# Kernel tuning notes

Measured on AMD Instinct MI355X. Metric: run time of the kernel, lower is better.

Reference implementation:

```python
import jax, jax.numpy as jnp
import numpy as np

N_NODES = 100000
N_EDGES = 3200000
D_IN = 256
D_OUT = 256


def setup_inputs() -> dict:
    key = jax.random.key(0)
    k1, k2, k3, k4, k5 = jax.random.split(key, 5)
    x = jax.random.normal(k1, (N_NODES, D_IN), dtype=jnp.float32)
    weight = jax.random.normal(k2, (D_IN, D_OUT), dtype=jnp.float32)
    edge_rows = jax.random.randint(k3, (N_EDGES,), 0, N_NODES, dtype=jnp.int32)
    edge_cols = jax.random.randint(k4, (N_EDGES,), 0, N_NODES, dtype=jnp.int32)
    edge_vals = jax.random.uniform(k5, (N_EDGES,), dtype=jnp.float32)
    return {"x": x, "weight": weight, "edge_rows": edge_rows,
            "edge_cols": edge_cols, "edge_vals": edge_vals}


def reference(x, weight, edge_rows, edge_cols, edge_vals):
    # GraphConvolution forward (eval mode, dense features, no bias):
    #   xw  = x @ W                      [N, D_OUT]
    #   out = relu(A_sparse @ xw)        A given as COO edge list
    xw = x @ weight  # [N, D_OUT]
    msgs = edge_vals[:, None] * xw[edge_cols]  # gather source features, scale
    agg = jax.ops.segment_sum(msgs, edge_rows, num_segments=N_NODES)
    return jax.nn.relu(agg)
```

## Files before the change

### kernel.cpp

```cpp
#include <hip/hip_runtime.h>
#include <hip/hip_bf16.h>

#define N_NODES 100000
#define N_EDGES 3200000
#define D 256
#define RSH 7
#define RPB 128
#define NB ((N_NODES + RPB - 1) / RPB)
#define FILL_CH 8192
#define NBLK_E ((N_EDGES + FILL_CH - 1) / FILL_CH)

typedef __attribute__((ext_vector_type(8))) short short8;
typedef __attribute__((ext_vector_type(4))) float floatx4;

__device__ __forceinline__ unsigned short f32_to_bf16_rne(float f) {
    unsigned int u = __float_as_uint(f);
    u += 0x7FFFu + ((u >> 16) & 1u);
    return (unsigned short)(u >> 16);
}
__device__ __forceinline__ float bf16_bits_to_f32(unsigned short b) {
    return __uint_as_float(((unsigned int)b) << 16);
}
__device__ __forceinline__ float blo(unsigned int x) { return __uint_as_float(x << 16); }
__device__ __forceinline__ float bhi(unsigned int x) { return __uint_as_float(x & 0xFFFF0000u); }

__global__ __launch_bounds__(256) void convert_w_k(const float* __restrict__ w,
                                                   unsigned short* __restrict__ wsw) {
    int t = blockIdx.x * 256 + threadIdx.x;
    int j     = t & 7;
    int lane  = (t >> 3) & 63;
    int kstep = (t >> 9) & 7;
    int ntile = t >> 12;
    int k = kstep * 32 + (lane >> 4) * 8 + j;
    int n = ntile * 16 + (lane & 15);
    wsw[t] = f32_to_bf16_rne(w[k * D + n]);
}

__global__ __launch_bounds__(256) void gemm_xw_k(const float* __restrict__ x,
                                                 const unsigned short* __restrict__ wsw,
                                                 unsigned short* __restrict__ xwb) {
    __shared__ uint4 wlds[8192];
    const int tid = threadIdx.x;
#pragma unroll
    for (int i = 0; i < 32; ++i) {
        int idx = i * 256 + tid;
        wlds[idx] = ((const uint4*)wsw)[idx];
    }
    __syncthreads();

    const int lane = tid & 63;
    const int wave = tid >> 6;
    const int q    = lane >> 4;
    const int ml   = lane & 15;
    const long rowBase = (long)blockIdx.x * 64 + wave * 16;
    long arow = rowBase + ml;
    if (arow >= N_NODES) arow = 0;
    const float* xr = x + arow * (long)D;

    floatx4 acc[16];
#pragma unroll
    for (int i = 0; i < 16; ++i) acc[i] = (floatx4){0.f, 0.f, 0.f, 0.f};

    const short8* wfrag = (const short8*)wlds;

#pragma unroll
    for (int ks = 0; ks < 8; ++ks) {
        const float4 a0 = *(const float4*)(xr + ks * 32 + q * 8);
        const float4 a1 = *(const float4*)(xr + ks * 32 + q * 8 + 4);
        short8 af;
        af[0] = (short)f32_to_bf16_rne(a0.x);
        af[1] = (short)f32_to_bf16_rne(a0.y);
        af[2] = (short)f32_to_bf16_rne(a0.z);
        af[3] = (short)f32_to_bf16_rne(a0.w);
        af[4] = (short)f32_to_bf16_rne(a1.x);
        af[5] = (short)f32_to_bf16_rne(a1.y);
        af[6] = (short)f32_to_bf16_rne(a1.z);
        af[7] = (short)f32_to_bf16_rne(a1.w);
#pragma unroll
        for (int nt = 0; nt < 16; ++nt) {
            acc[nt] = __builtin_amdgcn_mfma_f32_16x16x32_bf16(
                af, wfrag[(nt * 8 + ks) * 64 + lane], acc[nt], 0, 0, 0);
        }
    }

#pragma unroll
    for (int nt = 0; nt < 16; ++nt) {
#pragma unroll
        for (int r = 0; r < 4; ++r) {
            long orow = rowBase + q * 4 + r;
            if (orow < N_NODES)
                xwb[orow * (long)D + nt * 16 + ml] = f32_to_bf16_rne(acc[nt][r]);
        }
    }
}

__global__ __launch_bounds__(256) void zero_counts_k(int* __restrict__ counts) {
    int i = blockIdx.x * 256 + threadIdx.x;
    if (i < NB) counts[i] = 0;
}

__global__ __launch_bounds__(256) void bhist_k(const int* __restrict__ erow,
                                               int* __restrict__ counts) {
    __shared__ int h[NB];
    const int tid = threadIdx.x;
    for (int i = tid; i < NB; i += 256) h[i] = 0;
    __syncthreads();
    const int s = blockIdx.x * FILL_CH;
    const int e = min(s + FILL_CH, N_EDGES);
    for (int i = s + tid; i < e; i += 256) atomicAdd(&h[erow[i] >> RSH], 1);
    __syncthreads();
    for (int i = tid; i < NB; i += 256)
        if (h[i] > 0) atomicAdd(&counts[i], h[i]);
}

__global__ __launch_bounds__(1024) void bscan_k(const int* __restrict__ counts,
                                                int* __restrict__ bbase,
                                                int* __restrict__ bcursor) {
    __shared__ int sc[1024];
    const int t = threadIdx.x;
    int v = (t < NB) ? counts[t] : 0;
    sc[t] = v;
    __syncthreads();
    for (int o = 1; o < 1024; o <<= 1) {
        int add = (t >= o) ? sc[t - o] : 0;
        __syncthreads();
        sc[t] += add;
        __syncthreads();
    }
    int excl = sc[t] - v;
    if (t < NB) { bbase[t] = excl; bcursor[t] = excl; }
    if (t == NB - 1) bbase[NB] = sc[t];
}

__global__ __launch_bounds__(256) void binfill_k(const int* __restrict__ erow,
                                                 const int* __restrict__ ecol,
                                                 const float* __restrict__ eval,
                                                 int* __restrict__ bcursor,
                                                 unsigned long long* __restrict__ recs) {
    __shared__ int h[NB];
    __shared__ int lcur[NB];
    const int tid = threadIdx.x;
    for (int i = tid; i < NB; i += 256) h[i] = 0;
    __syncthreads();
    const int s = blockIdx.x * FILL_CH;
    const int e = min(s + FILL_CH, N_EDGES);
    for (int i = s + tid; i < e; i += 256) atomicAdd(&h[erow[i] >> RSH], 1);
    __syncthreads();
    for (int i = tid; i < NB; i += 256) {
        int cnt = h[i];
        lcur[i] = (cnt > 0) ? atomicAdd(&bcursor[i], cnt) : 0;
    }
    __syncthreads();
    for (int i = s + tid; i < e; i += 256) {
        int r = erow[i];
        int b = r >> RSH;
        int pos = atomicAdd(&lcur[b], 1);
        unsigned long long rec =
            ((unsigned long long)(r & (RPB - 1)) << 33) |
            ((unsigned long long)f32_to_bf16_rne(eval[i]) << 17) |
            (unsigned int)ecol[i];
        recs[pos] = rec;
    }
}

__global__ __launch_bounds__(256) void bsort_k(const int* __restrict__ bbase,
                                               const unsigned long long* __restrict__ recs,
                                               int* __restrict__ offsets,
                                               unsigned int* __restrict__ cs,
                                               unsigned short* __restrict__ vs) {
    __shared__ int hist[RPB];
    __shared__ int cur[RPB];
    __shared__ int sc[RPB];
    const int t = threadIdx.x;
    const int b = blockIdx.x;
    const int base = bbase[b];
    const int endp = bbase[b + 1];

    if (t < RPB) hist[t] = 0;
    __syncthreads();
    for (int i = base + t; i < endp; i += 256)
        atomicAdd(&hist[(int)(recs[i] >> 33)], 1);
    __syncthreads();

    if (t < RPB) sc[t] = hist[t];
    __syncthreads();
    for (int o = 1; o < RPB; o <<= 1) {
        int add = (t >= o && t < RPB) ? sc[t - o] : 0;
        __syncthreads();
        if (t < RPB) sc[t] += add;
        __syncthreads();
    }
    if (t < RPB) {
        int excl = sc[t] - hist[t];
        cur[t] = excl;
        int r = (b << RSH) + t;
        if (r <= N_NODES) offsets[r] = base + excl;
    }
    __syncthreads();

    for (int i = base + t; i < endp; i += 256) {
        unsigned long long rec = recs[i];
        int rl = (int)(rec >> 33);
        int pos = base + atomicAdd(&cur[rl], 1);
        cs[pos] = (unsigned int)(rec & 0x1FFFFu);
        vs[pos] = (unsigned short)((rec >> 17) & 0xFFFFu);
    }
}

__global__ __launch_bounds__(256) void aggregate_k(const unsigned short* __restrict__ xwb,
                                                   const int* __restrict__ offsets,
                                                   const unsigned int* __restrict__ cs,
                                                   const unsigned short* __restrict__ vs,
                                                   float* __restrict__ out) {
    const int wave = threadIdx.x >> 6;
    const int lane = threadIdx.x & 63;
    const int r = blockIdx.x * 4 + wave;
    if (r >= N_NODES) return;

    const int start = offsets[r];
    const int end   = offsets[r + 1];
    const int half  = lane >> 5;
    const int hl    = lane & 31;

    float acc[8];
#pragma unroll
    for (int k = 0; k < 8; ++k) acc[k] = 0.f;

    for (int jb = start; jb < end; jb += 64) {
        int j = jb + lane;
        unsigned int c = 0;
        float v = 0.f;
        if (j < end) {
            c = cs[j];
            v = bf16_bits_to_f32(vs[j]);
        }
        const int cnt = min(64, end - jb);
        const int pairs = (cnt + 1) >> 1;
        int t = 0;
        for (; t + 4 <= pairs; t += 4) {
            uint4 q0, q1, q2, q3;
            float b0, b1, b2, b3;
#define SLOT(s, qv, bv)                                                        \
            {                                                                  \
                int src = 2 * (t + (s)) + half;                                \
                int srcc = min(src, cnt - 1);                                  \
                unsigned int bc = (unsigned int)__shfl((int)c, srcc);          \
                float bb = __shfl(v, srcc);                                    \
                bv = (src < cnt) ? bb : 0.f;                                   \
                qv = ((const uint4*)(xwb + (size_t)bc * D))[hl];               \
            }
            SLOT(0, q0, b0)
            SLOT(1, q1, b1)
            SLOT(2, q2, b2)
            SLOT(3, q3, b3)
#undef SLOT
#define FMA8(qv, bv)                                                           \
            acc[0] += bv * blo(qv.x); acc[1] += bv * bhi(qv.x);                \
            acc[2] += bv * blo(qv.y); acc[3] += bv * bhi(qv.y);                \
            acc[4] += bv * blo(qv.z); acc[5] += bv * bhi(qv.z);                \
            acc[6] += bv * blo(qv.w); acc[7] += bv * bhi(qv.w);
            FMA8(q0, b0)
            FMA8(q1, b1)
            FMA8(q2, b2)
            FMA8(q3, b3)
#undef FMA8
        }
        for (; t < pairs; ++t) {
            int src = 2 * t + half;
            int srcc = min(src, cnt - 1);
            unsigned int bc = (unsigned int)__shfl((int)c, srcc);
            float bb = __shfl(v, srcc);
            float bv = (src < cnt) ? bb : 0.f;
            uint4 q = ((const uint4*)(xwb + (size_t)bc * D))[hl];
            acc[0] += bv * blo(q.x); acc[1] += bv * bhi(q.x);
            acc[2] += bv * blo(q.y); acc[3] += bv * bhi(q.y);
            acc[4] += bv * blo(q.z); acc[5] += bv * bhi(q.z);
            acc[6] += bv * blo(q.w); acc[7] += bv * bhi(q.w);
        }
    }

#pragma unroll
    for (int k = 0; k < 8; ++k) acc[k] += __shfl_xor(acc[k], 32);

    const int s = lane >> 1;
    const int par = lane & 1;
    float4 o;
    {
        float a0 = __shfl(acc[0], s), b0 = __shfl(acc[4], s);
        float a1 = __shfl(acc[1], s), b1 = __shfl(acc[5], s);
        float a2 = __shfl(acc[2], s), b2 = __shfl(acc[6], s);
        float a3 = __shfl(acc[3], s), b3 = __shfl(acc[7], s);
        o.x = par ? b0 : a0;
        o.y = par ? b1 : a1;
        o.z = par ? b2 : a2;
        o.w = par ? b3 : a3;
    }
    o.x = fmaxf(o.x, 0.f);
    o.y = fmaxf(o.y, 0.f);
    o.z = fmaxf(o.z, 0.f);
    o.w = fmaxf(o.w, 0.f);
    ((float4*)(out + (size_t)r * D))[lane] = o;
}

extern "C" void kernel_launch(void* const* d_in, const int* in_sizes, int n_in,
                              void* d_out, int out_size, void* d_ws, size_t ws_size,
                              hipStream_t stream) {
    const float* x    = (const float*)d_in[0];
    const float* w    = (const float*)d_in[1];
    const int*   erow = (const int*)d_in[2];
    const int*   ecol = (const int*)d_in[3];
    const float* eval = (const float*)d_in[4];
    float* out = (float*)d_out;

    char* p = (char*)d_ws;
    auto align = [](size_t v) { return (v + 255) & ~(size_t)255; };

    unsigned short* xwb = (unsigned short*)p;
    p += align((size_t)N_NODES * D * sizeof(unsigned short));
    unsigned short* wsw = (unsigned short*)p;
    p += align((size_t)D * D * sizeof(unsigned short));
    int* bcounts = (int*)p;  p += align((size_t)NB * sizeof(int));
    int* bbase   = (int*)p;  p += align((size_t)(NB + 1) * sizeof(int));
    int* bcursor = (int*)p;  p += align((size_t)NB * sizeof(int));
    unsigned long long* recs = (unsigned long long*)p;
    p += align((size_t)N_EDGES * sizeof(unsigned long long));
    unsigned int*   cs = (unsigned int*)p;    p += align((size_t)N_EDGES * 4);
    unsigned short* vs = (unsigned short*)p;  p += align((size_t)N_EDGES * 2);
    int* offsets = (int*)p;  p += align((size_t)(N_NODES + 1) * sizeof(int));

    convert_w_k<<<(D * D) / 256, 256, 0, stream>>>(w, wsw);
    gemm_xw_k<<<(N_NODES + 63) / 64, 256, 0, stream>>>(x, wsw, xwb);
    zero_counts_k<<<(NB + 255) / 256, 256, 0, stream>>>(bcounts);
    bhist_k<<<NBLK_E, 256, 0, stream>>>(erow, bcounts);
    bscan_k<<<1, 1024, 0, stream>>>(bcounts, bbase, bcursor);
    binfill_k<<<NBLK_E, 256, 0, stream>>>(erow, ecol, eval, bcursor, recs);
    bsort_k<<<NB, 256, 0, stream>>>(bbase, recs, offsets, cs, vs);
    aggregate_k<<<(N_NODES + 3) / 4, 256, 0, stream>>>(xwb, offsets, cs, vs, out);
}
```

Baseline: 609.7 us.

## Enlarge GEMM blocks, deepen aggregate gather unroll, replace zero kernel with memset

The GEMM kernel now runs 512-thread blocks covering 128 rows, so the 128 KB bf16 weight tile loaded into LDS is reused by twice as many waves. The aggregation inner loop now issues eight unmasked row gathers per iteration over full pairs, with a 4-wide step and a masked scalar tail, and the outer and inner loops are kept rolled. This aims for more loads in flight and less per-slot clamping and masking. The bucket-count zeroing kernel is replaced by hipMemsetAsync. The costs are higher register pressure in the aggregate loop and fewer GEMM blocks resident per CU because of the large LDS footprint.

```diff
diff --git a/kernel.cpp b/kernel.cpp
--- a/kernel.cpp
+++ b/kernel.cpp
@@ -36,14 +36,14 @@
     wsw[t] = f32_to_bf16_rne(w[k * D + n]);
 }
 
-__global__ __launch_bounds__(256) void gemm_xw_k(const float* __restrict__ x,
+__global__ __launch_bounds__(512) void gemm_xw_k(const float* __restrict__ x,
                                                  const unsigned short* __restrict__ wsw,
                                                  unsigned short* __restrict__ xwb) {
     __shared__ uint4 wlds[8192];
     const int tid = threadIdx.x;
 #pragma unroll
-    for (int i = 0; i < 32; ++i) {
-        int idx = i * 256 + tid;
+    for (int i = 0; i < 16; ++i) {
+        int idx = i * 512 + tid;
         wlds[idx] = ((const uint4*)wsw)[idx];
     }
     __syncthreads();
@@ -52,7 +52,7 @@
     const int wave = tid >> 6;
     const int q    = lane >> 4;
     const int ml   = lane & 15;
-    const long rowBase = (long)blockIdx.x * 64 + wave * 16;
+    const long rowBase = (long)blockIdx.x * 128 + wave * 16;
     long arow = rowBase + ml;
     if (arow >= N_NODES) arow = 0;
     const float* xr = x + arow * (long)D;
@@ -94,11 +94,6 @@
     }
 }
 
-__global__ __launch_bounds__(256) void zero_counts_k(int* __restrict__ counts) {
-    int i = blockIdx.x * 256 + threadIdx.x;
-    if (i < NB) counts[i] = 0;
-}
-
 __global__ __launch_bounds__(256) void bhist_k(const int* __restrict__ erow,
                                                int* __restrict__ counts) {
     __shared__ int h[NB];
@@ -226,6 +221,7 @@
 #pragma unroll
     for (int k = 0; k < 8; ++k) acc[k] = 0.f;
 
+#pragma unroll 1
     for (int jb = start; jb < end; jb += 64) {
         int j = jb + lane;
         unsigned int c = 0;
@@ -236,35 +232,41 @@
         }
         const int cnt = min(64, end - jb);
         const int pairs = (cnt + 1) >> 1;
+        const int hp = cnt >> 1;
         int t = 0;
-        for (; t + 4 <= pairs; t += 4) {
+
+#define FMA8(qv, bv)                                                           \
+        acc[0] += bv * blo(qv.x); acc[1] += bv * bhi(qv.x);                    \
+        acc[2] += bv * blo(qv.y); acc[3] += bv * bhi(qv.y);                    \
+        acc[4] += bv * blo(qv.z); acc[5] += bv * bhi(qv.z);                    \
+        acc[6] += bv * blo(qv.w); acc[7] += bv * bhi(qv.w);
+#define SLOTF(s, qv, bv)                                                       \
+        {                                                                      \
+            int src = 2 * (t + (s)) + half;                                    \
+            unsigned int bc = (unsigned int)__shfl((int)c, src);               \
+            bv = __shfl(v, src);                                               \
+            qv = ((const uint4*)(xwb + (size_t)bc * D))[hl];                   \
+        }
+
+#pragma unroll 1
+        for (; t + 8 <= hp; t += 8) {
+            uint4 q0, q1, q2, q3, q4, q5, q6, q7;
+            float b0, b1, b2, b3, b4, b5, b6, b7;
+            SLOTF(0, q0, b0) SLOTF(1, q1, b1) SLOTF(2, q2, b2) SLOTF(3, q3, b3)
+            SLOTF(4, q4, b4) SLOTF(5, q5, b5) SLOTF(6, q6, b6) SLOTF(7, q7, b7)
+            FMA8(q0, b0) FMA8(q1, b1) FMA8(q2, b2) FMA8(q3, b3)
+            FMA8(q4, b4) FMA8(q5, b5) FMA8(q6, b6) FMA8(q7, b7)
+        }
+        if (t + 4 <= hp) {
             uint4 q0, q1, q2, q3;
             float b0, b1, b2, b3;
-#define SLOT(s, qv, bv)                                                        \
-            {                                                                  \
-                int src = 2 * (t + (s)) + half;                                \
-                int srcc = min(src, cnt - 1);                                  \
-                unsigned int bc = (unsigned int)__shfl((int)c, srcc);          \
-                float bb = __shfl(v, srcc);                                    \
-                bv = (src < cnt) ? bb : 0.f;                                   \
-                qv = ((const uint4*)(xwb + (size_t)bc * D))[hl];               \
-            }
-            SLOT(0, q0, b0)
-            SLOT(1, q1, b1)
-            SLOT(2, q2, b2)
-            SLOT(3, q3, b3)
-#undef SLOT
-#define FMA8(qv, bv)                                                           \
-            acc[0] += bv * blo(qv.x); acc[1] += bv * bhi(qv.x);                \
-            acc[2] += bv * blo(qv.y); acc[3] += bv * bhi(qv.y);                \
-            acc[4] += bv * blo(qv.z); acc[5] += bv * bhi(qv.z);                \
-            acc[6] += bv * blo(qv.w); acc[7] += bv * bhi(qv.w);
-            FMA8(q0, b0)
-            FMA8(q1, b1)
-            FMA8(q2, b2)
-            FMA8(q3, b3)
-#undef FMA8
-        }
+            SLOTF(0, q0, b0) SLOTF(1, q1, b1) SLOTF(2, q2, b2) SLOTF(3, q3, b3)
+            FMA8(q0, b0) FMA8(q1, b1) FMA8(q2, b2) FMA8(q3, b3)
+            t += 4;
+        }
+#undef SLOTF
+
+#pragma unroll 1
         for (; t < pairs; ++t) {
             int src = 2 * t + half;
             int srcc = min(src, cnt - 1);
@@ -272,11 +274,9 @@
             float bb = __shfl(v, srcc);
             float bv = (src < cnt) ? bb : 0.f;
             uint4 q = ((const uint4*)(xwb + (size_t)bc * D))[hl];
-            acc[0] += bv * blo(q.x); acc[1] += bv * bhi(q.x);
-            acc[2] += bv * blo(q.y); acc[3] += bv * bhi(q.y);
-            acc[4] += bv * blo(q.z); acc[5] += bv * bhi(q.z);
-            acc[6] += bv * blo(q.w); acc[7] += bv * bhi(q.w);
-        }
+            FMA8(q, bv)
+        }
+#undef FMA8
     }
 
 #pragma unroll
@@ -329,8 +329,8 @@
     int* offsets = (int*)p;  p += align((size_t)(N_NODES + 1) * sizeof(int));
 
     convert_w_k<<<(D * D) / 256, 256, 0, stream>>>(w, wsw);
-    gemm_xw_k<<<(N_NODES + 63) / 64, 256, 0, stream>>>(x, wsw, xwb);
-    zero_counts_k<<<(NB + 255) / 256, 256, 0, stream>>>(bcounts);
+    gemm_xw_k<<<(N_NODES + 127) / 128, 512, 0, stream>>>(x, wsw, xwb);
+    hipMemsetAsync(bcounts, 0, (size_t)NB * sizeof(int), stream);
     bhist_k<<<NBLK_E, 256, 0, stream>>>(erow, bcounts);
     bscan_k<<<1, 1024, 0, stream>>>(bcounts, bbase, bcursor);
     binfill_k<<<NBLK_E, 256, 0, stream>>>(erow, ecol, eval, bcursor, recs);
```

After: 587.7 us. 3.6% less time.
